# Kernel optimization log

Measured on AMD Instinct MI355X. Metric: run time of the kernel, lower is better.

Reference implementation:

```python
import jax, jax.numpy as jnp
import numpy as np

B, T1, T2, D, O = 8, 64, 128, 512, 512

def setup_inputs() -> dict:
    key = jax.random.key(0)
    k1, k2, k3 = jax.random.split(key, 3)
    X = jax.random.normal(k1, (B, T1, T2, D), dtype=jnp.float32)
    W = jax.random.normal(k2, (D, O), dtype=jnp.float32) * (1.0 / np.sqrt(D))
    b = jax.random.normal(k3, (O,), dtype=jnp.float32) * 0.01
    return {"X": X, "W": W, "b": b}

def reference(X, W, b):
    # Original serializes this via nested K.rnn scans over time1/time2, but the
    # math is a single per-position dense + bias + tanh activation.
    # btsd,do->btso
    return jnp.tanh(jnp.einsum("btsd,do->btso", X, W) + b)
```

## Files before the change

kernel.cpp:

```cpp
#include <hip/hip_runtime.h>
#include <stdint.h>


typedef short bf16x8 __attribute__((ext_vector_type(8)));
typedef float f32x16 __attribute__((ext_vector_type(16)));

#define KTOT 512
#define NTOT 512
#define WT_BYTES   524288ull
#define WS_NEEDED  WT_BYTES

typedef __attribute__((address_space(3))) uint8_t lds8;
typedef __attribute__((address_space(1))) const uint8_t glb8;

__device__ __forceinline__ uint32_t pk2(float a, float b) {
  uint16_t lo = __builtin_bit_cast(uint16_t, (__bf16)a);
  uint16_t hi = __builtin_bit_cast(uint16_t, (__bf16)b);
  return (uint32_t)lo | ((uint32_t)hi << 16);
}

__device__ __forceinline__ float fast_tanh(float z) {
  float t = __builtin_amdgcn_exp2f(z * 2.8853900817779268f);
  return 1.0f - 2.0f * __builtin_amdgcn_rcpf(t + 1.0f);
}

__device__ __forceinline__ int swz4(int r) { return ((r >> 1) ^ (r >> 3)) & 3; }

__global__ __launch_bounds__(256)
void cvtW_kernel(const float* __restrict__ W, uint8_t* __restrict__ Wt) {
  const int c    = blockIdx.x * 256 + threadIdx.x;
  const int j    = c & 3;
  const int r    = (c >> 2) & 127;
  const int tile = c >> 9;
  const int s    = tile & 15;
  const int bn   = tile >> 4;
  const int n    = bn * 128 + r;
  const int k0   = s * 32 + j * 8;
  float e[8];
#pragma unroll
  for (int i = 0; i < 8; ++i) e[i] = W[(size_t)(k0 + i) * NTOT + n];
  uint4 v = make_uint4(pk2(e[0], e[1]), pk2(e[2], e[3]),
                       pk2(e[4], e[5]), pk2(e[6], e[7]));
  *(uint4*)(Wt + ((size_t)tile << 13) + (r << 6) + ((j ^ swz4(r)) << 4)) = v;
}

__global__ __launch_bounds__(256, 3)
void hotdd_fused(const float* __restrict__ X, const uint8_t* __restrict__ Wt,
                 const float* __restrict__ Bv, float* __restrict__ Y) {
  __shared__ uint8_t Ab0[8192], Ab1[8192], Bb0[8192], Bb1[8192];

  const int d  = blockIdx.x;
  const int bm = ((d >> 5) << 3) | (d & 7);
  const int bn = (d >> 3) & 3;

  const int tid  = threadIdx.x;
  const int lane = tid & 63;
  const int wv   = tid >> 6;
  const int wr   = (wv >> 1) * 64;
  const int wc   = (wv & 1) * 64;
  const int lo5  = lane & 31;
  const int hi1  = lane >> 5;

  const int arow  = wv * 32 + (lane >> 1);
  const int ahalf = lane & 1;
  const float* pA = X + (size_t)(bm * 128 + arow) * KTOT + ahalf * 16;
  const int ak  = swz4(arow);
  const int aw0 = arow * 64 + ((((ahalf << 1) | 0) ^ ak) << 4);
  const int aw1 = arow * 64 + ((((ahalf << 1) | 1) ^ ak) << 4);

  const uint8_t* pB = Wt + ((size_t)(bn * 16) << 13) + wv * 2048 + lane * 16;
  uint8_t* Bd0 = Bb0 + wv * 2048;
  uint8_t* Bd1 = Bb1 + wv * 2048;

  const int rA0 = wr + lo5, rA1 = rA0 + 32;
  const int rB0 = wc + lo5, rB1 = rB0 + 32;
  const int oA0 = rA0 * 64, oA1 = rA1 * 64;
  const int oB0 = rB0 * 64, oB1 = rB1 * 64;
  const int kA0 = swz4(rA0), kA1 = swz4(rA1);
  const int kB0 = swz4(rB0), kB1 = swz4(rB1);

  float4 ra0, ra1, ra2, ra3;
  float4 rb0, rb1, rb2, rb3;
  f32x16 acc00 = {}, acc01 = {}, acc10 = {}, acc11 = {};

#define SEP() asm volatile("" ::: "memory")
#define VM(N)  asm volatile("s_waitcnt vmcnt(" #N ")" ::: "memory")
#define LGKM0() asm volatile("s_waitcnt lgkmcnt(0)" ::: "memory")

#define BGLDS(BD, S) do {                                                     \
    const uint8_t* bs_ = pB + ((size_t)(S) << 13);                            \
    __builtin_amdgcn_global_load_lds((glb8*)bs_, (lds8*)(BD), 16, 0, 0);      \
    __builtin_amdgcn_global_load_lds((glb8*)(bs_ + 1024),                     \
                                     (lds8*)((BD) + 1024), 16, 0, 0);         \
    SEP();                                                                    \
  } while (0)

#define LOADA(R0, R1, R2, R3, S) do {                                         \
    const float* ap_ = pA + (S) * 32;                                         \
    R0 = *(const float4*)(ap_ + 0);  R1 = *(const float4*)(ap_ + 4);          \
    R2 = *(const float4*)(ap_ + 8);  R3 = *(const float4*)(ap_ + 12);         \
    SEP();                                                                    \
  } while (0)

#define CVTA(R0, R1, R2, R3, AB) do {                                         \
    *(uint4*)((AB) + aw0) = make_uint4(pk2(R0.x, R0.y), pk2(R0.z, R0.w),      \
                                       pk2(R1.x, R1.y), pk2(R1.z, R1.w));     \
    *(uint4*)((AB) + aw1) = make_uint4(pk2(R2.x, R2.y), pk2(R2.z, R2.w),      \
                                       pk2(R3.x, R3.y), pk2(R3.z, R3.w));     \
  } while (0)

#define MFMA_STEP(AB, BB) do {                                                \
    _Pragma("unroll")                                                         \
    for (int kk = 0; kk < 2; ++kk) {                                          \
      const int c_ = (kk << 1) | hi1;                                         \
      bf16x8 fa0 = *(const bf16x8*)((AB) + oA0 + ((c_ ^ kA0) << 4));          \
      bf16x8 fa1 = *(const bf16x8*)((AB) + oA1 + ((c_ ^ kA1) << 4));          \
      bf16x8 fb0 = *(const bf16x8*)((BB) + oB0 + ((c_ ^ kB0) << 4));          \
      bf16x8 fb1 = *(const bf16x8*)((BB) + oB1 + ((c_ ^ kB1) << 4));          \
      acc00 = __builtin_amdgcn_mfma_f32_32x32x16_bf16(fa0, fb0, acc00, 0,0,0);\
      acc01 = __builtin_amdgcn_mfma_f32_32x32x16_bf16(fa0, fb1, acc01, 0,0,0);\
      acc10 = __builtin_amdgcn_mfma_f32_32x32x16_bf16(fa1, fb0, acc10, 0,0,0);\
      acc11 = __builtin_amdgcn_mfma_f32_32x32x16_bf16(fa1, fb1, acc11, 0,0,0);\
    }                                                                         \
  } while (0)

  LOADA(ra0, ra1, ra2, ra3, 0);
  BGLDS(Bd0, 0);
  LOADA(rb0, rb1, rb2, rb3, 1);
  VM(6);
  CVTA(ra0, ra1, ra2, ra3, Ab0);
  LGKM0();

#pragma unroll 1
  for (int t = 0; t < 14; t += 2) {
    VM(4);
    __builtin_amdgcn_s_barrier();
    BGLDS(Bd1, t + 1);
    LOADA(ra0, ra1, ra2, ra3, t + 2);
    MFMA_STEP(Ab0, Bb0);
    VM(6);
    CVTA(rb0, rb1, rb2, rb3, Ab1);
    LGKM0();
    VM(4);
    __builtin_amdgcn_s_barrier();
    BGLDS(Bd0, t + 2);
    LOADA(rb0, rb1, rb2, rb3, t + 3);
    MFMA_STEP(Ab1, Bb1);
    VM(6);
    CVTA(ra0, ra1, ra2, ra3, Ab0);
    LGKM0();
  }

  VM(4);
  __builtin_amdgcn_s_barrier();
  BGLDS(Bd1, 15);
  MFMA_STEP(Ab0, Bb0);
  VM(2);
  CVTA(rb0, rb1, rb2, rb3, Ab1);
  LGKM0();
  VM(0);
  __builtin_amdgcn_s_barrier();
  MFMA_STEP(Ab1, Bb1);

  const int gn0 = bn * 128 + wc + lo5;
  const int gn1 = gn0 + 32;
  const float bv0 = Bv[gn0];
  const float bv1 = Bv[gn1];

#define EPI(ACC, MI, GN, BVAL) do {                                           \
    _Pragma("unroll")                                                         \
    for (int r = 0; r < 16; ++r) {                                            \
      const int mloc = wr + (MI) * 32 + (hi1 << 2) + ((r >> 2) << 3) + (r & 3);\
      Y[(size_t)(bm * 128 + mloc) * NTOT + (GN)] = fast_tanh((ACC)[r] + (BVAL));\
    }                                                                         \
  } while (0)

  EPI(acc00, 0, gn0, bv0);
  EPI(acc01, 0, gn1, bv1);
  EPI(acc10, 1, gn0, bv0);
  EPI(acc11, 1, gn1, bv1);
}

struct Regs {
  float4 a0,a1,a2,a3,a4,a5,a6,a7;
  float4 u0,u1,u2,u3;
  float4 v0,v1,v2,v3;
};

__global__ __launch_bounds__(256, 2)
void hotdd_fallback(const float* __restrict__ X, const float* __restrict__ W,
                    const float* __restrict__ Bv, float* __restrict__ Y) {
  __shared__ char Ab[128 * 64 * 2];
  __shared__ char Bb[128 * 64 * 2];
  const int d  = blockIdx.x;
  const int bm = ((d >> 5) << 3) | (d & 7);
  const int bn = (d >> 3) & 3;
  const int tid  = threadIdx.x;
  const int lane = tid & 63;
  const int wv   = tid >> 6;
  const int wr   = (wv >> 1) * 64;
  const int wc   = (wv & 1) * 64;
  const int lo5  = lane & 31;
  const int hi1  = lane >> 5;
  const int rs   = lo5 & 7;
  const int am   = tid >> 1;
  const int ah   = tid & 1;
  const int amz  = am & 7;
  const int abase = am * 128;
  const float* Ag = X + (size_t)(bm * 128 + am) * KTOT + ah * 32;
  const int kp = lo5;
  const int ng = wv * 32 + hi1 * 16;
  const float* Bg = W + (size_t)(2 * kp) * NTOT + bn * 128 + ng;

#define LOADR(R, K0) do {                                                     \
    const float* ap_ = Ag + (K0);                                             \
    R.a0 = *(const float4*)(ap_ +  0); R.a1 = *(const float4*)(ap_ +  4);     \
    R.a2 = *(const float4*)(ap_ +  8); R.a3 = *(const float4*)(ap_ + 12);     \
    R.a4 = *(const float4*)(ap_ + 16); R.a5 = *(const float4*)(ap_ + 20);     \
    R.a6 = *(const float4*)(ap_ + 24); R.a7 = *(const float4*)(ap_ + 28);     \
    const float* bp_ = Bg + (size_t)(K0) * NTOT;                              \
    R.u0 = *(const float4*)(bp_ +  0); R.u1 = *(const float4*)(bp_ +  4);     \
    R.u2 = *(const float4*)(bp_ +  8); R.u3 = *(const float4*)(bp_ + 12);     \
    R.v0 = *(const float4*)(bp_ + NTOT +  0); R.v1 = *(const float4*)(bp_ + NTOT +  4); \
    R.v2 = *(const float4*)(bp_ + NTOT +  8); R.v3 = *(const float4*)(bp_ + NTOT + 12); \
  } while (0)

#define ASTF(R, J, P, Q)                                                      \
    *(uint4*)(Ab + abase + (((((ah << 2) + (J)) ^ amz)) << 4)) =              \
      make_uint4(pk2(R.P.x, R.P.y), pk2(R.P.z, R.P.w),                        \
                 pk2(R.Q.x, R.Q.y), pk2(R.Q.z, R.Q.w));
#define BSTF(R, I, UV, C)                                                     \
    *(uint32_t*)(Bb + (ng + (I)) * 128 + ((kp << 2) ^ (((I) & 7) << 4))) =    \
      pk2(R.u##UV.C, R.v##UV.C);

#define STORERF(R) do {                                                       \
    ASTF(R, 0, a0, a1) ASTF(R, 1, a2, a3) ASTF(R, 2, a4, a5) ASTF(R, 3, a6, a7)\
    BSTF(R, 0, 0, x) BSTF(R, 1, 0, y) BSTF(R, 2, 0, z) BSTF(R, 3, 0, w)       \
    BSTF(R, 4, 1, x) BSTF(R, 5, 1, y) BSTF(R, 6, 1, z) BSTF(R, 7, 1, w)       \
    BSTF(R, 8, 2, x) BSTF(R, 9, 2, y) BSTF(R,10, 2, z) BSTF(R,11, 2, w)       \
    BSTF(R,12, 3, x) BSTF(R,13, 3, y) BSTF(R,14, 3, z) BSTF(R,15, 3, w)       \
  } while (0)

  f32x16 acc00 = {}, acc01 = {}, acc10 = {}, acc11 = {};
  const char* Ard0 = Ab + (wr + lo5) * 128;
  const char* Ard1 = Ard0 + 32 * 128;
  const char* Brd0 = Bb + (wc + lo5) * 128;
  const char* Brd1 = Brd0 + 32 * 128;

#define MFMA_PHASE_F() do {                                                   \
    _Pragma("unroll")                                                         \
    for (int kk = 0; kk < 4; ++kk) {                                          \
      const int sb = ((((kk << 1) | hi1) ^ rs) << 4);                         \
      bf16x8 fa0 = *(const bf16x8*)(Ard0 + sb);                               \
      bf16x8 fa1 = *(const bf16x8*)(Ard1 + sb);                               \
      bf16x8 fb0 = *(const bf16x8*)(Brd0 + sb);                               \
      bf16x8 fb1 = *(const bf16x8*)(Brd1 + sb);                               \
      acc00 = __builtin_amdgcn_mfma_f32_32x32x16_bf16(fa0, fb0, acc00, 0,0,0);\
      acc01 = __builtin_amdgcn_mfma_f32_32x32x16_bf16(fa0, fb1, acc01, 0,0,0);\
      acc10 = __builtin_amdgcn_mfma_f32_32x32x16_bf16(fa1, fb0, acc10, 0,0,0);\
      acc11 = __builtin_amdgcn_mfma_f32_32x32x16_bf16(fa1, fb1, acc11, 0,0,0);\
    }                                                                         \
  } while (0)

  Regs r0, r1;
  LOADR(r0, 0);
#pragma unroll 1
  for (int s = 0; s < 8; s += 2) {
    STORERF(r0);
    __syncthreads();
    LOADR(r1, (s + 1) * 64);
    MFMA_PHASE_F();
    __syncthreads();
    STORERF(r1);
    __syncthreads();
    if (s + 2 < 8) LOADR(r0, (s + 2) * 64);
    MFMA_PHASE_F();
    __syncthreads();
  }

  const int gn0 = bn * 128 + wc + lo5;
  const int gn1 = gn0 + 32;
  const float bv0 = Bv[gn0];
  const float bv1 = Bv[gn1];
  EPI(acc00, 0, gn0, bv0);
  EPI(acc01, 0, gn1, bv1);
  EPI(acc10, 1, gn0, bv0);
  EPI(acc11, 1, gn1, bv1);
}

extern "C" void kernel_launch(void* const* d_in, const int* in_sizes, int n_in,
                              void* d_out, int out_size, void* d_ws, size_t ws_size,
                              hipStream_t stream) {
  (void)in_sizes; (void)n_in; (void)out_size;
  const float* X = (const float*)d_in[0];
  const float* W = (const float*)d_in[1];
  const float* b = (const float*)d_in[2];
  float* Y = (float*)d_out;
  if (ws_size >= WS_NEEDED) {
    uint8_t* Wt = (uint8_t*)d_ws;
    hipLaunchKernelGGL(cvtW_kernel, dim3(128),  dim3(256), 0, stream, W, Wt);
    hipLaunchKernelGGL(hotdd_fused, dim3(2048), dim3(256), 0, stream, X, Wt, b, Y);
  } else {
    hipLaunchKernelGGL(hotdd_fallback, dim3(2048), dim3(256), 0, stream, X, W, b, Y);
  }
}
```

Before: 78.39 us.

## Triple-buffer LDS tiles to prefetch W two stages ahead

Adds a third LDS buffer for both the A and B tiles and restructures the main loop into a six-step rotation. The B tile for stage t+2 is issued while stage t computes, which gives the direct-to-LDS loads more latency slack and removes the vmcnt wait before each barrier. LDS use per block rises from 32KB to 48KB, which may reduce occupancy under launch_bounds(256,3). The reworked wait counts also need to stay correct for every stage.

```diff
diff --git a/kernel.cpp b/kernel.cpp
--- a/kernel.cpp
+++ b/kernel.cpp
@@ -47,7 +47,8 @@
 __global__ __launch_bounds__(256, 3)
 void hotdd_fused(const float* __restrict__ X, const uint8_t* __restrict__ Wt,
                  const float* __restrict__ Bv, float* __restrict__ Y) {
-  __shared__ uint8_t Ab0[8192], Ab1[8192], Bb0[8192], Bb1[8192];
+  __shared__ uint8_t Ab0[8192], Ab1[8192], Ab2[8192];
+  __shared__ uint8_t Bb0[8192], Bb1[8192], Bb2[8192];
 
   const int d  = blockIdx.x;
   const int bm = ((d >> 5) << 3) | (d & 7);
@@ -69,8 +70,6 @@
   const int aw1 = arow * 64 + ((((ahalf << 1) | 1) ^ ak) << 4);
 
   const uint8_t* pB = Wt + ((size_t)(bn * 16) << 13) + wv * 2048 + lane * 16;
-  uint8_t* Bd0 = Bb0 + wv * 2048;
-  uint8_t* Bd1 = Bb1 + wv * 2048;
 
   const int rA0 = wr + lo5, rA1 = rA0 + 32;
   const int rB0 = wc + lo5, rB1 = rB0 + 32;
@@ -89,9 +88,11 @@
 
 #define BGLDS(BD, S) do {                                                     \
     const uint8_t* bs_ = pB + ((size_t)(S) << 13);                            \
-    __builtin_amdgcn_global_load_lds((glb8*)bs_, (lds8*)(BD), 16, 0, 0);      \
+    __builtin_amdgcn_global_load_lds((glb8*)bs_,                              \
+                                     (lds8*)((BD) + wv * 2048), 16, 0, 0);    \
     __builtin_amdgcn_global_load_lds((glb8*)(bs_ + 1024),                     \
-                                     (lds8*)((BD) + 1024), 16, 0, 0);         \
+                                     (lds8*)((BD) + wv * 2048 + 1024),        \
+                                     16, 0, 0);                               \
     SEP();                                                                    \
   } while (0)
 
@@ -124,43 +125,43 @@
     }                                                                         \
   } while (0)
 
+#define STEPX(T, ABC, BBC, ABW, BBW, L0,L1,L2,L3, C0,C1,C2,C3) do {           \
+    __builtin_amdgcn_s_barrier();                                             \
+    BGLDS(BBW, (T) + 2);                                                      \
+    LOADA(L0, L1, L2, L3, (T) + 2);                                           \
+    MFMA_STEP(ABC, BBC);                                                      \
+    VM(6);                                                                    \
+    CVTA(C0, C1, C2, C3, ABW);                                                \
+    LGKM0();                                                                  \
+  } while (0)
+
+  BGLDS(Bb0, 0);
   LOADA(ra0, ra1, ra2, ra3, 0);
-  BGLDS(Bd0, 0);
+  BGLDS(Bb1, 1);
   LOADA(rb0, rb1, rb2, rb3, 1);
   VM(6);
   CVTA(ra0, ra1, ra2, ra3, Ab0);
   LGKM0();
 
 #pragma unroll 1
-  for (int t = 0; t < 14; t += 2) {
-    VM(4);
-    __builtin_amdgcn_s_barrier();
-    BGLDS(Bd1, t + 1);
-    LOADA(ra0, ra1, ra2, ra3, t + 2);
-    MFMA_STEP(Ab0, Bb0);
-    VM(6);
-    CVTA(rb0, rb1, rb2, rb3, Ab1);
-    LGKM0();
-    VM(4);
-    __builtin_amdgcn_s_barrier();
-    BGLDS(Bd0, t + 2);
-    LOADA(rb0, rb1, rb2, rb3, t + 3);
-    MFMA_STEP(Ab1, Bb1);
-    VM(6);
-    CVTA(ra0, ra1, ra2, ra3, Ab0);
-    LGKM0();
+  for (int t = 0; t < 12; t += 6) {
+    STEPX(t + 0, Ab0, Bb0, Ab1, Bb2, ra0,ra1,ra2,ra3, rb0,rb1,rb2,rb3);
+    STEPX(t + 1, Ab1, Bb1, Ab2, Bb0, rb0,rb1,rb2,rb3, ra0,ra1,ra2,ra3);
+    STEPX(t + 2, Ab2, Bb2, Ab0, Bb1, ra0,ra1,ra2,ra3, rb0,rb1,rb2,rb3);
+    STEPX(t + 3, Ab0, Bb0, Ab1, Bb2, rb0,rb1,rb2,rb3, ra0,ra1,ra2,ra3);
+    STEPX(t + 4, Ab1, Bb1, Ab2, Bb0, ra0,ra1,ra2,ra3, rb0,rb1,rb2,rb3);
+    STEPX(t + 5, Ab2, Bb2, Ab0, Bb1, rb0,rb1,rb2,rb3, ra0,ra1,ra2,ra3);
   }
-
-  VM(4);
+  STEPX(12, Ab0, Bb0, Ab1, Bb2, ra0,ra1,ra2,ra3, rb0,rb1,rb2,rb3);
+  STEPX(13, Ab1, Bb1, Ab2, Bb0, rb0,rb1,rb2,rb3, ra0,ra1,ra2,ra3);
+
   __builtin_amdgcn_s_barrier();
-  BGLDS(Bd1, 15);
+  MFMA_STEP(Ab2, Bb2);
+  VM(0);
+  CVTA(rb0, rb1, rb2, rb3, Ab0);
+  LGKM0();
+  __builtin_amdgcn_s_barrier();
   MFMA_STEP(Ab0, Bb0);
-  VM(2);
-  CVTA(rb0, rb1, rb2, rb3, Ab1);
-  LGKM0();
-  VM(0);
-  __builtin_amdgcn_s_barrier();
-  MFMA_STEP(Ab1, Bb1);
 
   const int gn0 = bn * 128 + wc + lo5;
   const int gn1 = gn0 + 32;
```

Measured after the change: 81.25 us. +3.6%, slower.
